# Performance work log

Hardware: AMD Instinct MI355X
Metric: run time of the kernel (lower is better)

## Reference

```python
import jax, jax.numpy as jnp
import numpy as np

KEEP_RATIO = 0.7

def setup_inputs() -> dict:
    key = jax.random.key(0)
    k1, k2, k3 = jax.random.split(key, 3)
    B, N, D = 4, 16384, 1024
    H = D // 4
    x = jax.random.normal(k1, (B, N, D), dtype=jnp.float32)
    W1 = jax.random.normal(k2, (D, H), dtype=jnp.float32) * (1.0 / np.sqrt(D))
    b1 = jnp.zeros((H,), dtype=jnp.float32)
    W2 = jax.random.normal(k3, (H, 1), dtype=jnp.float32) * (1.0 / np.sqrt(H))
    b2 = jnp.zeros((1,), dtype=jnp.float32)
    return {"x": x, "W1": W1, "b1": b1, "W2": W2, "b2": b2}

def reference(x, W1, b1, W2, b2):
    # x: [B, N, D]
    B, N, D = x.shape
    k = int(N * KEEP_RATIO)  # static under jit
    h = jax.nn.relu(jnp.einsum('bnd,dh->bnh', x, W1) + b1)
    scores = jax.nn.sigmoid(jnp.einsum('bnh,ho->bno', h, W2) + b2)  # [B, N, 1]
    score_values = scores[..., 0]  # [B, N]
    x_weighted = x * scores  # [B, N, D]
    _, top_k_indices = jax.lax.top_k(score_values, k)  # [B, k]
    top_k_indices = jnp.sort(top_k_indices, axis=1)
    x_kept = jnp.take_along_axis(x_weighted, top_k_indices[:, :, None], axis=1)  # [B, k, D]
    sparsity_loss = -jnp.mean(jnp.abs(score_values - 0.5))
    return x_kept, sparsity_loss
```

## Files before the change

kernel.cpp:

```cpp
#include <hip/hip_runtime.h>
#include <hip/hip_bf16.h>
#include <math.h>

#define N_TOK 16384
#define BATCH 4
#define DIM   1024
#define HID   256
#define KEEP  11468
#define MROWS 65536
#define BK    32
#define NKT   (DIM / BK)
#define DELTA 6e-3f
#define WCAP  4096
#define AP    40

typedef __attribute__((ext_vector_type(8))) short bf16x8;
typedef __attribute__((ext_vector_type(4))) float f32x4;

__device__ inline unsigned bf16_rne(float f) {
    unsigned u = __float_as_uint(f);
    return (u + 0x7FFFu + ((u >> 16) & 1u)) >> 16;
}

#define GLDS16(gp, lp) __builtin_amdgcn_global_load_lds( \
    (const __attribute__((address_space(1))) void*)(gp), \
    (__attribute__((address_space(3))) void*)(lp), 16, 0, 0)

__global__ __launch_bounds__(256) void prep_kernel(
    const float* __restrict__ W1, ushort* __restrict__ Wpk)
{
    const int kt = blockIdx.x;
    for (int idx = threadIdx.x; idx < 2048; idx += 256) {
        const int lane = idx & 63;
        const int g    = idx >> 6;
        const int h    = (g & 15) * 16 + (lane & 15);
        const int kb   = kt * 64 + (g >> 4) * 32 + (lane >> 4) * 8;
        ushort v[8];
#pragma unroll
        for (int j = 0; j < 8; ++j)
            v[j] = (ushort)bf16_rne(W1[(size_t)(kb + j) * HID + h]);
        *(uint4*)(Wpk + ((size_t)(kt * 32 + g) * 64 + lane) * 8) = *(uint4*)v;
    }
}

__global__ __launch_bounds__(512, 4) void score_mfma(
    const float* __restrict__ x, const ushort* __restrict__ Wpk,
    const float* __restrict__ b1, const float* __restrict__ W2,
    const float* __restrict__ b2, float* __restrict__ scores,
    float* __restrict__ partials)
{
    __shared__ ushort As[2][128 * AP];
    __shared__ ushort Bs[2][16 * 512];
    __shared__ float zbuf[128][4];
    __shared__ float red[128];

    const int t    = threadIdx.x;
    const int lane = t & 63;
    const int w    = t >> 6;
    const int wr   = w >> 2;
    const int wc   = w & 3;
    const int l15  = lane & 15;
    const int lk   = lane >> 4;
    const size_t row0 = (size_t)blockIdx.x * 128;

    const int arow = t >> 2;
    const int aq   = t & 3;
    const float* xbase = x + (row0 + arow) * DIM + aq * 8;

    f32x4 acc[4][4];
#pragma unroll
    for (int rf = 0; rf < 4; ++rf)
#pragma unroll
        for (int cf = 0; cf < 4; ++cf) acc[rf][cf] = (f32x4){0.f, 0.f, 0.f, 0.f};

    float pf[8];
#define LOADA(KT) { const float* xp = xbase + (KT) * BK; \
        *(float4*)&pf[0] = ((const float4*)xp)[0]; \
        *(float4*)&pf[4] = ((const float4*)xp)[1]; }
#define STOREA(BUF) { \
        ushort hb[8]; \
        _Pragma("unroll") \
        for (int j = 0; j < 8; ++j) hb[j] = (ushort)bf16_rne(pf[j]); \
        *(uint4*)&As[BUF][arow * AP + aq * 8] = *(uint4*)&hb[0]; }
#define LOADB(KT, BUF) { \
        _Pragma("unroll") \
        for (int i = 0; i < 2; ++i) { \
            const int g_ = w * 2 + i; \
            GLDS16(Wpk + (((size_t)(KT) * 16 + g_) * 64 + lane) * 8, \
                   &Bs[BUF][g_ * 512 + lane * 8]); \
        } }

    LOADB(0, 0);
    LOADA(0);
    STOREA(0);
    __syncthreads();

    for (int kt = 0; kt < NKT; ++kt) {
        const int cur = kt & 1;
        const int nxt = cur ^ 1;
        if (kt < NKT - 1) {
            LOADB(kt + 1, nxt);
            LOADA(kt + 1);
        }
        bf16x8 Af[4];
#pragma unroll
        for (int rf = 0; rf < 4; ++rf) {
            const int row = wr * 64 + rf * 16 + l15;
            Af[rf] = *(const bf16x8*)&As[cur][row * AP + lk * 8];
        }
#pragma unroll
        for (int cf = 0; cf < 4; ++cf) {
            const bf16x8 Bf = *(const bf16x8*)&Bs[cur][(wc * 4 + cf) * 512 + lane * 8];
            acc[0][cf] = __builtin_amdgcn_mfma_f32_16x16x32_bf16(Af[0], Bf, acc[0][cf], 0, 0, 0);
            acc[1][cf] = __builtin_amdgcn_mfma_f32_16x16x32_bf16(Af[1], Bf, acc[1][cf], 0, 0, 0);
            acc[2][cf] = __builtin_amdgcn_mfma_f32_16x16x32_bf16(Af[2], Bf, acc[2][cf], 0, 0, 0);
            acc[3][cf] = __builtin_amdgcn_mfma_f32_16x16x32_bf16(Af[3], Bf, acc[3][cf], 0, 0, 0);
        }
        if (kt < NKT - 1) STOREA(nxt);
        __syncthreads();
    }

    float b1r[4], w2r[4];
#pragma unroll
    for (int cf = 0; cf < 4; ++cf) {
        const int col = wc * 64 + cf * 16 + l15;
        b1r[cf] = b1[col];
        w2r[cf] = W2[col];
    }
#pragma unroll
    for (int rf = 0; rf < 4; ++rf) {
#pragma unroll
        for (int j = 0; j < 4; ++j) {
            float z = 0.f;
#pragma unroll
            for (int cf = 0; cf < 4; ++cf)
                z = fmaf(fmaxf(acc[rf][cf][j] + b1r[cf], 0.f), w2r[cf], z);
            z += __shfl_xor(z, 1);
            z += __shfl_xor(z, 2);
            z += __shfl_xor(z, 4);
            z += __shfl_xor(z, 8);
            if (l15 == 0) zbuf[wr * 64 + rf * 16 + lk * 4 + j][wc] = z;
        }
    }
    __syncthreads();
    if (t < 128) {
        const float z = (zbuf[t][0] + zbuf[t][1]) + (zbuf[t][2] + zbuf[t][3]) + b2[0];
        const float s = 1.f / (1.f + expf(-z));
        scores[row0 + t] = s;
        red[t] = fabsf(s - 0.5f);
    }
    __syncthreads();
    for (int off = 64; off > 0; off >>= 1) {
        if (t < off) red[t] += red[t + off];
        __syncthreads();
    }
    if (t == 0) partials[blockIdx.x] = red[0];
}

__global__ __launch_bounds__(1024) void fixfind_kernel(
    const float* __restrict__ scores, int* __restrict__ winList,
    int* __restrict__ winCnt)
{
    const int b    = blockIdx.x;
    const int t    = threadIdx.x;
    const int lane = t & 63;
    const int wid  = t >> 6;
    __shared__ unsigned red[17];
    __shared__ unsigned wsum[16];

    float sv[16];
    unsigned bits[16];
    const float4* sp = (const float4*)(scores + (size_t)b * N_TOK + t * 16);
#pragma unroll
    for (int j = 0; j < 4; ++j) {
        const float4 v = sp[j];
        sv[j * 4 + 0] = v.x; sv[j * 4 + 1] = v.y;
        sv[j * 4 + 2] = v.z; sv[j * 4 + 3] = v.w;
    }
#pragma unroll
    for (int j = 0; j < 16; ++j) bits[j] = __float_as_uint(sv[j]);

    auto countGE = [&](unsigned v) -> unsigned {
        unsigned c = 0;
#pragma unroll
        for (int j = 0; j < 16; ++j) c += (bits[j] >= v) ? 1u : 0u;
        c += __shfl_xor(c, 32); c += __shfl_xor(c, 16); c += __shfl_xor(c, 8);
        c += __shfl_xor(c, 4);  c += __shfl_xor(c, 2);  c += __shfl_xor(c, 1);
        if (lane == 0) red[wid] = c;
        __syncthreads();
        if (t == 0) {
            unsigned s = 0;
            for (int w = 0; w < 16; ++w) s += red[w];
            red[16] = s;
        }
        __syncthreads();
        return red[16];
    };

    unsigned lo = 0u, hi = 0x40000000u;
    while (hi - lo > 1u) {
        const unsigned mid = (lo + hi) >> 1;
        if (countGE(mid) >= KEEP) lo = mid; else hi = mid;
    }
    const float sT = __uint_as_float(lo);

    int cnt = 0;
    bool inw[16];
#pragma unroll
    for (int j = 0; j < 16; ++j) {
        inw[j] = fabsf(sv[j] - sT) <= DELTA;
        cnt += inw[j] ? 1 : 0;
    }
    unsigned inc = (unsigned)cnt;
#pragma unroll
    for (int off = 1; off < 64; off <<= 1) {
        const unsigned n = __shfl_up(inc, off);
        if (lane >= off) inc += n;
    }
    const unsigned excl = inc - (unsigned)cnt;
    if (lane == 63) wsum[wid] = inc;
    __syncthreads();
    if (t == 0) {
        unsigned s = 0;
        for (int w = 0; w < 16; ++w) { const unsigned tmp = wsum[w]; wsum[w] = s; s += tmp; }
        winCnt[b] = (int)(s > WCAP ? WCAP : s);
    }
    __syncthreads();
    unsigned pos = wsum[wid] + excl;
#pragma unroll
    for (int j = 0; j < 16; ++j) {
        if (inw[j]) {
            if (pos < WCAP) winList[b * WCAP + pos] = t * 16 + j;
            ++pos;
        }
    }
}

__global__ __launch_bounds__(1024) void fix2_kernel(
    const float* __restrict__ x, const float* __restrict__ W1,
    const float* __restrict__ b1, const float* __restrict__ W2,
    const float* __restrict__ b2, float* __restrict__ scores,
    const int* __restrict__ winList, const int* __restrict__ winCnt)
{
    __shared__ float xrT[1024][8];
    __shared__ float part[4][8][256];
    __shared__ int rows[8];

    const int t = threadIdx.x;
    int c[4], cum[5];
    cum[0] = 0;
    for (int b = 0; b < 4; ++b) {
        int cc = winCnt[b];
        if (cc > WCAP) cc = WCAP;
        if (cc < 0) cc = 0;
        c[b] = cc;
        cum[b + 1] = cum[b] + ((cc + 7) >> 3);
    }
    for (int g = blockIdx.x; g < cum[4]; g += gridDim.x) {
        int b = 0;
        while (g >= cum[b + 1]) ++b;
        const int gi   = g - cum[b];
        const int nval = min(8, c[b] - gi * 8);
        if (t < 8)
            rows[t] = winList[b * WCAP + gi * 8 + (t < nval ? t : 0)];
        __syncthreads();
        {
            const int r = t >> 7, c0 = (t & 127) * 8;
            const float* xp = x + ((size_t)b * N_TOK + rows[r]) * DIM + c0;
            const float4 a = ((const float4*)xp)[0], bq = ((const float4*)xp)[1];
            xrT[c0 + 0][r] = a.x;  xrT[c0 + 1][r] = a.y;
            xrT[c0 + 2][r] = a.z;  xrT[c0 + 3][r] = a.w;
            xrT[c0 + 4][r] = bq.x; xrT[c0 + 5][r] = bq.y;
            xrT[c0 + 6][r] = bq.z; xrT[c0 + 7][r] = bq.w;
        }
        __syncthreads();
        const int h = t & 255, q = t >> 8;
        float a8[8];
#pragma unroll
        for (int r = 0; r < 8; ++r) a8[r] = 0.f;
        const int k0 = q * 256;
        for (int k = 0; k < 256; ++k) {
            const float wv = W1[(size_t)(k0 + k) * HID + h];
            const float4 xa = *(const float4*)&xrT[k0 + k][0];
            const float4 xb = *(const float4*)&xrT[k0 + k][4];
            a8[0] = fmaf(xa.x, wv, a8[0]); a8[1] = fmaf(xa.y, wv, a8[1]);
            a8[2] = fmaf(xa.z, wv, a8[2]); a8[3] = fmaf(xa.w, wv, a8[3]);
            a8[4] = fmaf(xb.x, wv, a8[4]); a8[5] = fmaf(xb.y, wv, a8[5]);
            a8[6] = fmaf(xb.z, wv, a8[6]); a8[7] = fmaf(xb.w, wv, a8[7]);
        }
#pragma unroll
        for (int r = 0; r < 8; ++r) part[q][r][h] = a8[r];
        __syncthreads();
        const int wid = t >> 6, lane = t & 63;
        if (wid < 8) {
            const int r = wid;
            float v = 0.f;
#pragma unroll
            for (int i = 0; i < 4; ++i) {
                const int hc = i * 64 + lane;
                float hv = (part[0][r][hc] + part[1][r][hc]) + (part[2][r][hc] + part[3][r][hc]);
                hv = fmaxf(hv + b1[hc], 0.f);
                v = fmaf(hv, W2[hc], v);
            }
            v += __shfl_xor(v, 32); v += __shfl_xor(v, 16); v += __shfl_xor(v, 8);
            v += __shfl_xor(v, 4);  v += __shfl_xor(v, 2);  v += __shfl_xor(v, 1);
            if (lane == 0 && r < nval)
                scores[(size_t)b * N_TOK + rows[r]] = 1.f / (1.f + expf(-(v + b2[0])));
        }
        __syncthreads();
    }
}

__global__ __launch_bounds__(1024) void select_kernel(
    const float* __restrict__ scores, int* __restrict__ idxList)
{
    const int b    = blockIdx.x;
    const int t    = threadIdx.x;
    const int lane = t & 63;
    const int wid  = t >> 6;
    __shared__ unsigned red[17];

    unsigned bits[16];
    const float4* sp = (const float4*)(scores + (size_t)b * N_TOK + t * 16);
#pragma unroll
    for (int j = 0; j < 4; ++j) {
        const float4 v = sp[j];
        bits[j * 4 + 0] = __float_as_uint(v.x);
        bits[j * 4 + 1] = __float_as_uint(v.y);
        bits[j * 4 + 2] = __float_as_uint(v.z);
        bits[j * 4 + 3] = __float_as_uint(v.w);
    }

    auto countGE = [&](unsigned v) -> unsigned {
        unsigned c = 0;
#pragma unroll
        for (int j = 0; j < 16; ++j) c += (bits[j] >= v) ? 1u : 0u;
        c += __shfl_xor(c, 32); c += __shfl_xor(c, 16); c += __shfl_xor(c, 8);
        c += __shfl_xor(c, 4);  c += __shfl_xor(c, 2);  c += __shfl_xor(c, 1);
        if (lane == 0) red[wid] = c;
        __syncthreads();
        if (t == 0) {
            unsigned s = 0;
            for (int w = 0; w < 16; ++w) s += red[w];
            red[16] = s;
        }
        __syncthreads();
        return red[16];
    };

    unsigned lo = 0u, hi = 0x40000000u;
    while (hi - lo > 1u) {
        const unsigned mid = (lo + hi) >> 1;
        if (countGE(mid) >= KEEP) lo = mid; else hi = mid;
    }
    const unsigned T    = lo;
    const unsigned cGT  = countGE(T + 1u);
    const unsigned need = KEEP - cGT;

    unsigned pre[16];
    unsigned run = 0;
#pragma unroll
    for (int j = 0; j < 16; ++j) {
        pre[j] = run;
        const unsigned gt = (bits[j] > T) ? 1u : 0u;
        const unsigned eq = (bits[j] == T) ? 1u : 0u;
        run += gt | (eq << 16);
    }
    unsigned inc = run;
#pragma unroll
    for (int off = 1; off < 64; off <<= 1) {
        const unsigned n = __shfl_up(inc, off);
        if (lane >= off) inc += n;
    }
    const unsigned waveExcl = inc - run;
    if (lane == 63) red[wid] = inc;
    __syncthreads();
    if (t == 0) {
        unsigned s = 0;
        for (int w = 0; w < 16; ++w) { const unsigned tmp = red[w]; red[w] = s; s += tmp; }
    }
    __syncthreads();
    const unsigned base = red[wid] + waveExcl;

#pragma unroll
    for (int j = 0; j < 16; ++j) {
        const unsigned pe    = base + pre[j];
        const unsigned tieR  = pe >> 16;
        const unsigned posGT = pe & 0xFFFFu;
        const bool gt = bits[j] > T;
        const bool eq = bits[j] == T;
        if (gt || (eq && tieR < need)) {
            const unsigned pos = posGT + (tieR < need ? tieR : need);
            idxList[(size_t)b * KEEP + pos] = t * 16 + j;
        }
    }
}

__global__ __launch_bounds__(256) void gather_kernel(
    const float* __restrict__ x, const float* __restrict__ scores,
    const int* __restrict__ idxList, float* __restrict__ out)
{
    const int t = threadIdx.x;
#pragma unroll
    for (int q = 0; q < 4; ++q) {
        const int orow = blockIdx.x * 4 + q;
        const int b    = orow / KEEP;
        const int idx  = idxList[orow];
        const float s  = scores[(size_t)b * N_TOK + idx];
        const float4 v = *(const float4*)(x + (((size_t)b * N_TOK + idx) << 10) + t * 4);
        float4 o;
        o.x = v.x * s; o.y = v.y * s; o.z = v.z * s; o.w = v.w * s;
        *(float4*)(out + ((size_t)orow << 10) + t * 4) = o;
    }
}

__global__ __launch_bounds__(256) void loss_kernel(
    const float* __restrict__ partials, float* __restrict__ outLoss)
{
    __shared__ float red[256];
    const int t = threadIdx.x;
    red[t] = partials[t] + partials[t + 256];
    __syncthreads();
    for (int off = 128; off > 0; off >>= 1) {
        if (t < off) red[t] += red[t + off];
        __syncthreads();
    }
    if (t == 0) outLoss[0] = -(red[0] / (float)MROWS);
}

extern "C" void kernel_launch(void* const* d_in, const int* in_sizes, int n_in,
                              void* d_out, int out_size, void* d_ws, size_t ws_size,
                              hipStream_t stream)
{
    const float* x  = (const float*)d_in[0];
    const float* W1 = (const float*)d_in[1];
    const float* b1 = (const float*)d_in[2];
    const float* W2 = (const float*)d_in[3];
    const float* b2 = (const float*)d_in[4];
    float* out = (float*)d_out;

    char* ws = (char*)d_ws;
    float* scores   = (float*)ws;
    float* partials = (float*)(ws + 262144);
    int*   idxList  = (int*)(ws + 266240);
    ushort* Wpk     = (ushort*)(ws + 458752);
    int*   winList  = (int*)(ws + 983040);
    int*   winCnt   = (int*)(ws + 1048576);

    prep_kernel<<<16, 256, 0, stream>>>(W1, Wpk);
    score_mfma<<<MROWS / 128, 512, 0, stream>>>(x, Wpk, b1, W2, b2, scores, partials);
    loss_kernel<<<1, 256, 0, stream>>>(partials, out + (size_t)BATCH * KEEP * DIM);
    fixfind_kernel<<<BATCH, 1024, 0, stream>>>(scores, winList, winCnt);
    fix2_kernel<<<256, 1024, 0, stream>>>(x, W1, b1, W2, b2, scores, winList, winCnt);
    select_kernel<<<BATCH, 1024, 0, stream>>>(scores, idxList);
    gather_kernel<<<KEEP, 256, 0, stream>>>(x, scores, idxList, out);
}
```

Measured before the change: 229.4 us.

## Triple-buffer score GEMM with two-stage-ahead x prefetch and manual waitcnt barriers

The score GEMM moves from double to triple LDS buffering. x tiles are prefetched two k-steps ahead into alternating register sets, and each iteration uses explicit vmcnt/lgkmcnt waits with raw s_barrier instead of __syncthreads, so global loads overlap the MFMA work with one barrier per step. The epilogue scratch arrays now alias the B buffer to keep LDS usage in check. Separately, the 16-way count reduction in the binary-search kernels is done with a wavefront shuffle instead of a serial loop on thread 0. The hand-written waitcnt counts add correctness risk, and the larger LDS footprint may reduce occupancy.

```diff
diff --git a/kernel.cpp b/kernel.cpp
--- a/kernel.cpp
+++ b/kernel.cpp
@@ -13,6 +13,8 @@
 #define DELTA 6e-3f
 #define WCAP  4096
 #define AP    40
+#define ASLOT (128 * AP)
+#define BSLOT (16 * 512)
 
 typedef __attribute__((ext_vector_type(8))) short bf16x8;
 typedef __attribute__((ext_vector_type(4))) float f32x4;
@@ -49,10 +51,8 @@
     const float* __restrict__ b2, float* __restrict__ scores,
     float* __restrict__ partials)
 {
-    __shared__ ushort As[2][128 * AP];
-    __shared__ ushort Bs[2][16 * 512];
-    __shared__ float zbuf[128][4];
-    __shared__ float red[128];
+    __shared__ ushort AsAll[3 * ASLOT];
+    __shared__ ushort BsAll[3 * BSLOT];
 
     const int t    = threadIdx.x;
     const int lane = t & 63;
@@ -73,53 +73,71 @@
 #pragma unroll
         for (int cf = 0; cf < 4; ++cf) acc[rf][cf] = (f32x4){0.f, 0.f, 0.f, 0.f};
 
-    float pf[8];
-#define LOADA(KT) { const float* xp = xbase + (KT) * BK; \
-        *(float4*)&pf[0] = ((const float4*)xp)[0]; \
-        *(float4*)&pf[4] = ((const float4*)xp)[1]; }
-#define STOREA(BUF) { \
+    float4 p0a, p0b, p1a, p1b;
+
+#define ISSUEA(KT, PA, PB) { \
+        const float4* xp = (const float4*)(xbase + (size_t)(KT) * BK); \
+        PA = xp[0]; PB = xp[1]; }
+#define CONVA(PA, PB, SLOT) { \
         ushort hb[8]; \
-        _Pragma("unroll") \
-        for (int j = 0; j < 8; ++j) hb[j] = (ushort)bf16_rne(pf[j]); \
-        *(uint4*)&As[BUF][arow * AP + aq * 8] = *(uint4*)&hb[0]; }
-#define LOADB(KT, BUF) { \
+        hb[0] = (ushort)bf16_rne(PA.x); hb[1] = (ushort)bf16_rne(PA.y); \
+        hb[2] = (ushort)bf16_rne(PA.z); hb[3] = (ushort)bf16_rne(PA.w); \
+        hb[4] = (ushort)bf16_rne(PB.x); hb[5] = (ushort)bf16_rne(PB.y); \
+        hb[6] = (ushort)bf16_rne(PB.z); hb[7] = (ushort)bf16_rne(PB.w); \
+        *(uint4*)&AsAll[(SLOT) * ASLOT + arow * AP + aq * 8] = *(uint4*)&hb[0]; }
+#define ISSUEB(KT, SLOT) { \
         _Pragma("unroll") \
         for (int i = 0; i < 2; ++i) { \
             const int g_ = w * 2 + i; \
             GLDS16(Wpk + (((size_t)(KT) * 16 + g_) * 64 + lane) * 8, \
-                   &Bs[BUF][g_ * 512 + lane * 8]); \
+                   &BsAll[(SLOT) * BSLOT + g_ * 512 + lane * 8]); \
         } }
-
-    LOADB(0, 0);
-    LOADA(0);
-    STOREA(0);
-    __syncthreads();
+#define COMPUTE(SLOT) { \
+        bf16x8 Af[4]; \
+        _Pragma("unroll") \
+        for (int rf = 0; rf < 4; ++rf) { \
+            const int row = wr * 64 + rf * 16 + l15; \
+            Af[rf] = *(const bf16x8*)&AsAll[(SLOT) * ASLOT + row * AP + lk * 8]; \
+        } \
+        _Pragma("unroll") \
+        for (int cf = 0; cf < 4; ++cf) { \
+            const bf16x8 Bf = *(const bf16x8*)&BsAll[(SLOT) * BSLOT + (wc * 4 + cf) * 512 + lane * 8]; \
+            acc[0][cf] = __builtin_amdgcn_mfma_f32_16x16x32_bf16(Af[0], Bf, acc[0][cf], 0, 0, 0); \
+            acc[1][cf] = __builtin_amdgcn_mfma_f32_16x16x32_bf16(Af[1], Bf, acc[1][cf], 0, 0, 0); \
+            acc[2][cf] = __builtin_amdgcn_mfma_f32_16x16x32_bf16(Af[2], Bf, acc[2][cf], 0, 0, 0); \
+            acc[3][cf] = __builtin_amdgcn_mfma_f32_16x16x32_bf16(Af[3], Bf, acc[3][cf], 0, 0, 0); \
+        } }
+
+    ISSUEB(0, 0);
+    ISSUEA(0, p0a, p0b);
+    ISSUEA(1, p1a, p1b);
+    CONVA(p0a, p0b, 0);
+    asm volatile("s_waitcnt lgkmcnt(0)" ::: "memory");
+    __builtin_amdgcn_s_barrier();
+    __builtin_amdgcn_sched_barrier(0);
 
     for (int kt = 0; kt < NKT; ++kt) {
-        const int cur = kt & 1;
-        const int nxt = cur ^ 1;
+        if (kt < NKT - 2) {
+            if ((kt & 1) == 0) { ISSUEA(kt + 2, p0a, p0b); }
+            else               { ISSUEA(kt + 2, p1a, p1b); }
+        }
         if (kt < NKT - 1) {
-            LOADB(kt + 1, nxt);
-            LOADA(kt + 1);
-        }
-        bf16x8 Af[4];
-#pragma unroll
-        for (int rf = 0; rf < 4; ++rf) {
-            const int row = wr * 64 + rf * 16 + l15;
-            Af[rf] = *(const bf16x8*)&As[cur][row * AP + lk * 8];
-        }
-#pragma unroll
-        for (int cf = 0; cf < 4; ++cf) {
-            const bf16x8 Bf = *(const bf16x8*)&Bs[cur][(wc * 4 + cf) * 512 + lane * 8];
-            acc[0][cf] = __builtin_amdgcn_mfma_f32_16x16x32_bf16(Af[0], Bf, acc[0][cf], 0, 0, 0);
-            acc[1][cf] = __builtin_amdgcn_mfma_f32_16x16x32_bf16(Af[1], Bf, acc[1][cf], 0, 0, 0);
-            acc[2][cf] = __builtin_amdgcn_mfma_f32_16x16x32_bf16(Af[2], Bf, acc[2][cf], 0, 0, 0);
-            acc[3][cf] = __builtin_amdgcn_mfma_f32_16x16x32_bf16(Af[3], Bf, acc[3][cf], 0, 0, 0);
-        }
-        if (kt < NKT - 1) STOREA(nxt);
-        __syncthreads();
-    }
-
+            const int s1 = (kt + 1) % 3;
+            ISSUEB(kt + 1, s1);
+            if ((kt & 1) == 0) { CONVA(p1a, p1b, s1); }
+            else               { CONVA(p0a, p0b, s1); }
+        }
+        if (kt < NKT - 2)       asm volatile("s_waitcnt vmcnt(4)" ::: "memory");
+        else if (kt == NKT - 2) asm volatile("s_waitcnt vmcnt(2)" ::: "memory");
+        else                    asm volatile("s_waitcnt vmcnt(0)" ::: "memory");
+        asm volatile("s_waitcnt lgkmcnt(0)" ::: "memory");
+        __builtin_amdgcn_s_barrier();
+        __builtin_amdgcn_sched_barrier(0);
+        COMPUTE(kt % 3);
+    }
+
+    float* zb = (float*)&BsAll[0];
+    float* rd = (float*)&BsAll[1024];
     float b1r[4], w2r[4];
 #pragma unroll
     for (int cf = 0; cf < 4; ++cf) {
@@ -139,22 +157,22 @@
             z += __shfl_xor(z, 2);
             z += __shfl_xor(z, 4);
             z += __shfl_xor(z, 8);
-            if (l15 == 0) zbuf[wr * 64 + rf * 16 + lk * 4 + j][wc] = z;
+            if (l15 == 0) zb[(wr * 64 + rf * 16 + lk * 4 + j) * 4 + wc] = z;
         }
     }
     __syncthreads();
     if (t < 128) {
-        const float z = (zbuf[t][0] + zbuf[t][1]) + (zbuf[t][2] + zbuf[t][3]) + b2[0];
+        const float z = (zb[t * 4 + 0] + zb[t * 4 + 1]) + (zb[t * 4 + 2] + zb[t * 4 + 3]) + b2[0];
         const float s = 1.f / (1.f + expf(-z));
         scores[row0 + t] = s;
-        red[t] = fabsf(s - 0.5f);
+        rd[t] = fabsf(s - 0.5f);
     }
     __syncthreads();
     for (int off = 64; off > 0; off >>= 1) {
-        if (t < off) red[t] += red[t + off];
-        __syncthreads();
-    }
-    if (t == 0) partials[blockIdx.x] = red[0];
+        if (t < off) rd[t] += rd[t + off];
+        __syncthreads();
+    }
+    if (t == 0) partials[blockIdx.x] = rd[0];
 }
 
 __global__ __launch_bounds__(1024) void fixfind_kernel(
@@ -188,10 +206,11 @@
         c += __shfl_xor(c, 4);  c += __shfl_xor(c, 2);  c += __shfl_xor(c, 1);
         if (lane == 0) red[wid] = c;
         __syncthreads();
-        if (t == 0) {
-            unsigned s = 0;
-            for (int w = 0; w < 16; ++w) s += red[w];
-            red[16] = s;
+        if (wid == 0) {
+            unsigned s = (lane < 16) ? red[lane] : 0u;
+            s += __shfl_xor(s, 8); s += __shfl_xor(s, 4);
+            s += __shfl_xor(s, 2); s += __shfl_xor(s, 1);
+            if (lane == 0) red[16] = s;
         }
         __syncthreads();
         return red[16];
@@ -339,10 +358,11 @@
         c += __shfl_xor(c, 4);  c += __shfl_xor(c, 2);  c += __shfl_xor(c, 1);
         if (lane == 0) red[wid] = c;
         __syncthreads();
-        if (t == 0) {
-            unsigned s = 0;
-            for (int w = 0; w < 16; ++w) s += red[w];
-            red[16] = s;
+        if (wid == 0) {
+            unsigned s = (lane < 16) ? red[lane] : 0u;
+            s += __shfl_xor(s, 8); s += __shfl_xor(s, 4);
+            s += __shfl_xor(s, 2); s += __shfl_xor(s, 1);
+            if (lane == 0) red[16] = s;
         }
         __syncthreads();
         return red[16];
```

New measurement: 227.7 us. About the same (-0.7%).
